# Kernel optimization log

Measured on AMD Instinct MI355X. Metric: run time of the kernel, lower is better.

The kernel has to match this reference:

```python
import jax, jax.numpy as jnp
import numpy as np

EPS = 1e-5

def layer_norm(x, g, b):
    mu = jnp.mean(x, axis=-1, keepdims=True)
    var = jnp.var(x, axis=-1, keepdims=True)
    return (x - mu) * jax.lax.rsqrt(var + EPS) * g + b

def rel_shift(x):
    # x: [N, H, T1, T2] with T2 = 2*T1 - 1 -> [N, H, T1, T1]
    N, H, T1, T2 = x.shape
    zp = jnp.zeros((N, H, T1, 1), dtype=x.dtype)
    xp = jnp.concatenate([zp, x], axis=-1).reshape(N, H, T2 + 1, T1)
    x = xp[:, :, 1:, :].reshape(N, H, T1, T2)
    return x[:, :, :, : T2 // 2 + 1]

def setup_inputs() -> dict:
    B, T, D, Hh = 8, 1024, 512, 8
    dk = D // Hh
    P = 2 * T - 1
    key = jax.random.key(0)
    ks = jax.random.split(key, 12)
    s = 0.02
    return {
        "q": jax.random.normal(ks[0], (B, T, D), jnp.float32),
        "k": jax.random.normal(ks[1], (B, T, D), jnp.float32),
        "v": jax.random.normal(ks[2], (B, T, D), jnp.float32),
        "pos_emb": jax.random.normal(ks[3], (1, P, D), jnp.float32),
        "mask": jnp.ones((B, T, T), jnp.int32),
        "ln_q_g": jnp.ones((D,), jnp.float32), "ln_q_b": jnp.zeros((D,), jnp.float32),
        "ln_k_g": jnp.ones((D,), jnp.float32), "ln_k_b": jnp.zeros((D,), jnp.float32),
        "ln_v_g": jnp.ones((D,), jnp.float32), "ln_v_b": jnp.zeros((D,), jnp.float32),
        "w_q": jax.random.normal(ks[4], (D, D), jnp.float32) * s,   # [out, in]
        "w_k": jax.random.normal(ks[5], (D, D), jnp.float32) * s,
        "w_v": jax.random.normal(ks[6], (D, D), jnp.float32) * s,
        "w_pos": jax.random.normal(ks[7], (D, D), jnp.float32) * s,
        "w_fc": jax.random.normal(ks[8], (D, D), jnp.float32) * s,
        "pos_bias_u": jax.random.normal(ks[9], (Hh, dk), jnp.float32) * s,
        "pos_bias_v": jax.random.normal(ks[10], (Hh, dk), jnp.float32) * s,
    }

def reference(q, k, v, pos_emb, mask, ln_q_g, ln_q_b, ln_k_g, ln_k_b, ln_v_g, ln_v_b,
              w_q, w_k, w_v, w_pos, w_fc, pos_bias_u, pos_bias_v):
    B, T, D = q.shape
    H, dk = pos_bias_u.shape
    scale = 1.0 / np.sqrt(dk).astype(np.float32)
    residual = q
    qn = layer_norm(q, ln_q_g, ln_q_b)
    kn = layer_norm(k, ln_k_g, ln_k_b)
    vn = layer_norm(v, ln_v_g, ln_v_b)
    # projections (torch Linear: x @ W^T), reshape to [B, H, T, dk]
    qh = (qn @ w_q.T).reshape(B, T, H, dk)                      # [B, T, H, dk]
    kh = (kn @ w_k.T).reshape(B, T, H, dk).transpose(0, 2, 1, 3)  # [B, H, T, dk]
    vh = (vn @ w_v.T).reshape(B, T, H, dk).transpose(0, 2, 1, 3)
    p = (pos_emb @ w_pos.T).reshape(pos_emb.shape[0], -1, H, dk).transpose(0, 2, 1, 3)  # [1, H, P, dk]
    q_u = (qh + pos_bias_u).transpose(0, 2, 1, 3)  # [B, H, T, dk]
    q_v = (qh + pos_bias_v).transpose(0, 2, 1, 3)
    matrix_ac = jnp.einsum('bhqd,bhkd->bhqk', q_u, kh)          # [B, H, T, T]
    matrix_bd = jnp.einsum('bhqd,nhpd->bhqp', q_v, p)           # [B, H, T, 2T-1]
    matrix_bd = rel_shift(matrix_bd)                             # [B, H, T, T]
    scores = (matrix_ac + matrix_bd) * scale
    m = (mask[:, None, :, :] == 0)                               # [B, 1, T, T]
    scores = jnp.where(m, -jnp.inf, scores)
    attn = jax.nn.softmax(scores, axis=-1)
    attn = jnp.where(m, 0.0, attn)
    out = jnp.einsum('bhqk,bhkd->bhqd', attn, vh)                # [B, H, T, dk]
    out = out.transpose(0, 2, 1, 3).reshape(B, T, H * dk)
    out = out @ w_fc.T + residual
    return out, attn
```

## Files before the change

### kernel.cpp

```cpp
#include <hip/hip_runtime.h>

constexpr int cT  = 1024;
constexpr int cD  = 512;
constexpr int cDK = 64;
constexpr int cP  = 2047;
constexpr int PBS = 1040;

typedef __attribute__((ext_vector_type(8))) short short8;
typedef __attribute__((ext_vector_type(4))) float floatx4;

#define MFMA16(a,b,c) __builtin_amdgcn_mfma_f32_16x16x32_bf16((a),(b),(c),0,0,0)
#define SWZ(i,j) ((j) ^ ((((i) >> 2) & 3) << 3))

__device__ __forceinline__ void bar_lds(){
  asm volatile("s_waitcnt lgkmcnt(0)\n\ts_barrier" ::: "memory");
}

__device__ __forceinline__ unsigned short f2bf(float f){
  union { float f; unsigned int u; } x; x.f = f;
  unsigned int r = x.u + 0x7fffu + ((x.u >> 16) & 1u);
  return (unsigned short)(r >> 16);
}
__device__ __forceinline__ float bf2f(unsigned short h){
  union { unsigned int u; float f; } x; x.u = ((unsigned int)h) << 16;
  return x.f;
}
__device__ __forceinline__ short8 ld8(const unsigned short* p){
  return *(const short8*)p;
}

struct LN3 { const float* x[3]; const float* g[3]; const float* b[3]; unsigned short* y[3]; };
__global__ void __launch_bounds__(256) ln3_kernel(LN3 a)
{
  __shared__ float red[8];
  const int z = blockIdx.y, r = blockIdx.x;
  const float* x = a.x[z]; const float* g = a.g[z]; const float* b = a.b[z];
  unsigned short* y = a.y[z];
  const float2 v = ((const float2*)(x + (size_t)r * cD))[threadIdx.x];
  float s = v.x + v.y, sq = v.x * v.x + v.y * v.y;
  #pragma unroll
  for (int o = 32; o; o >>= 1){ s += __shfl_xor(s, o); sq += __shfl_xor(sq, o); }
  const int w = threadIdx.x >> 6;
  if ((threadIdx.x & 63) == 0){ red[w * 2] = s; red[w * 2 + 1] = sq; }
  __syncthreads();
  s  = red[0] + red[2] + red[4] + red[6];
  sq = red[1] + red[3] + red[5] + red[7];
  const float mu  = s * (1.0f / cD);
  const float var = sq * (1.0f / cD) - mu * mu;
  const float rs  = rsqrtf(var + 1e-5f);
  const int c = threadIdx.x * 2;
  const unsigned int o0 = f2bf((v.x - mu) * rs * g[c]     + b[c]);
  const unsigned int o1 = f2bf((v.y - mu) * rs * g[c + 1] + b[c + 1]);
  ((unsigned int*)(y + (size_t)r * cD))[threadIdx.x] = o0 | (o1 << 16);
}

struct Ptr5 { const float* p[5]; };
__global__ void __launch_bounds__(256) cast5_kernel(Ptr5 s, unsigned short* __restrict__ d){
  const int idx = blockIdx.x * 256 + threadIdx.x;
  const int seg = idx >> 18, off = idx & 262143;
  d[idx] = f2bf(s.p[seg][off]);
}
__global__ void __launch_bounds__(256) cast1_kernel(const float* __restrict__ s,
    unsigned short* __restrict__ d, int n){
  const int idx = blockIdx.x * 256 + threadIdx.x;
  if (idx < n) d[idx] = f2bf(s[idx]);
}

__global__ void __launch_bounds__(256) maskbits_kernel(
    const int* __restrict__ mask, unsigned int* __restrict__ bm)
{
  const int row = blockIdx.x * 4 + (threadIdx.x >> 6);
  const int lane = threadIdx.x & 63;
  #pragma unroll
  for (int ii = 0; ii < 16; ii++){
    const int m = mask[(size_t)row * cT + ii * 64 + lane];
    const unsigned long long bal = __ballot(m != 0);
    if (lane == 0)       bm[row * 32 + ii * 2]     = (unsigned int)bal;
    else if (lane == 32) bm[row * 32 + ii * 2 + 1] = (unsigned int)(bal >> 32);
  }
}

__global__ void __launch_bounds__(256) gemm512_kernel(
    const unsigned short* __restrict__ A0, const unsigned short* __restrict__ W0,
    int M, int mode, float scaleA, unsigned short* __restrict__ outb,
    float* __restrict__ outf, const float* __restrict__ residual)
{
  const int z = blockIdx.z;
  const unsigned short* A = A0 + (size_t)z * 4194304;
  const unsigned short* W = W0 + (size_t)z * 262144;
  unsigned short* outz = outb ? outb + (size_t)z * 4194304 : outb;
  const float sA = (z == 0) ? scaleA : 1.0f;
  const int n0 = blockIdx.x * 128, m0 = blockIdx.y * 128;
  const int wave = threadIdx.x >> 6, lane = threadIdx.x & 63;
  const int wr = wave >> 1, wc = wave & 1;
  const int l15 = lane & 15, lq = lane >> 4;
  const int mb = m0 + wr * 64, nb = n0 + wc * 64;
  floatx4 acc[4][4];
  #pragma unroll
  for (int i = 0; i < 4; i++)
    #pragma unroll
    for (int j = 0; j < 4; j++) acc[i][j] = (floatx4){0.f, 0.f, 0.f, 0.f};
  for (int k0 = 0; k0 < 512; k0 += 32){
    short8 af[4], bf[4];
    #pragma unroll
    for (int i = 0; i < 4; i++){
      int row = mb + i * 16 + l15; if (row >= M) row = M - 1;
      af[i] = ld8(A + (size_t)row * 512 + k0 + lq * 8);
      const int col = nb + i * 16 + l15;
      bf[i] = ld8(W + (size_t)col * 512 + k0 + lq * 8);
    }
    #pragma unroll
    for (int i = 0; i < 4; i++)
      #pragma unroll
      for (int j = 0; j < 4; j++)
        acc[i][j] = MFMA16(af[i], bf[j], acc[i][j]);
  }
  #pragma unroll
  for (int i = 0; i < 4; i++){
    #pragma unroll
    for (int j = 0; j < 4; j++){
      #pragma unroll
      for (int r = 0; r < 4; r++){
        const int row = mb + i * 16 + lq * 4 + r;
        const int col = nb + j * 16 + l15;
        if (row >= M) continue;
        const float val = acc[i][j][r] * sA;
        if (mode == 0){
          const int bb = row >> 10, t = row & 1023, h = col >> 6, d = col & 63;
          outz[(((size_t)(bb * 8 + h) * 1024 + t) << 6) + d] = f2bf(val);
        } else if (mode == 1){
          const int h = col >> 6, d = col & 63;
          outz[(((size_t)h * 2047 + row) << 6) + d] = f2bf(val);
        } else {
          const size_t idx = (size_t)row * 512 + col;
          outf[idx] = val + residual[idx];
        }
      }
    }
  }
}

__global__ void __launch_bounds__(256) transpose_v_kernel(
    const unsigned short* __restrict__ vh, unsigned short* __restrict__ vt)
{
  __shared__ unsigned short tile[64][65];
  const int bh = blockIdx.x, t0 = blockIdx.y * 64;
  const unsigned short* src = vh + ((size_t)bh * cT + t0) * cDK;
  #pragma unroll
  for (int i = 0; i < 16; i++){
    const int idx = threadIdx.x + i * 256;
    tile[idx >> 6][idx & 63] = src[idx];
  }
  __syncthreads();
  unsigned short* dst = vt + (size_t)bh * cDK * cT + t0;
  #pragma unroll
  for (int i = 0; i < 16; i++){
    const int idx = threadIdx.x + i * 256;
    const int d = idx >> 6, t = idx & 63;
    dst[(size_t)d * cT + t] = tile[t][d];
  }
}

__global__ void __launch_bounds__(256) dot_bias_kernel(
    const unsigned short* __restrict__ X, const float* __restrict__ bias,
    float* __restrict__ out, int rows, int hdiv, float scale)
{
  const int row = blockIdx.x * 4 + (threadIdx.x >> 6);
  const int lane = threadIdx.x & 63;
  if (row >= rows) return;
  const int h = (row / hdiv) & 7;
  float s = bf2f(X[(size_t)row * 64 + lane]) * bias[h * 64 + lane];
  #pragma unroll
  for (int o = 32; o; o >>= 1) s += __shfl_xor(s, o);
  if (lane == 0) out[row] = s * scale;
}

__global__ void __launch_bounds__(512, 4) attn_kernel(
    const unsigned short* __restrict__ qh, const unsigned short* __restrict__ kh,
    const unsigned short* __restrict__ vt, const unsigned short* __restrict__ pproj,
    const float* __restrict__ ubias, const float* __restrict__ vbias,
    const unsigned int* __restrict__ bm, float* __restrict__ attn_out,
    unsigned short* __restrict__ out_h)
{
  __shared__ float sc[16 * cT];
  unsigned short* pbuf = (unsigned short*)sc;
  const int bh = blockIdx.x, b = bh >> 3, h = bh & 7;
  const int q0 = blockIdx.y * 16;
  const int wave = threadIdx.x >> 6, lane = threadIdx.x & 63;
  const int l15 = lane & 15, lq = lane >> 4;
  const unsigned short* Q  = qh + (size_t)bh * cT * cDK;
  const unsigned short* Kp = kh + (size_t)bh * cT * cDK;
  const unsigned short* Pt = pproj + (size_t)h * cP * cDK;
  const float* ub = ubias + (size_t)bh * cT;
  const float* vb = vbias + (size_t)h * cP;

  const short8 qf0 = ld8(Q + (size_t)(q0 + l15) * cDK + lq * 8);
  const short8 qf1 = ld8(Q + (size_t)(q0 + l15) * cDK + 32 + lq * 8);

  for (int jt = wave; jt < 64; jt += 8){
    const short8 kf0 = ld8(Kp + (size_t)(jt * 16 + l15) * cDK + lq * 8);
    const short8 kf1 = ld8(Kp + (size_t)(jt * 16 + l15) * cDK + 32 + lq * 8);
    floatx4 acc = (floatx4){0.f, 0.f, 0.f, 0.f};
    acc = MFMA16(qf0, kf0, acc);
    acc = MFMA16(qf1, kf1, acc);
    const int jb = jt * 16 + l15;
    const float ubv = ub[jb];
    #pragma unroll
    for (int r = 0; r < 4; r++){
      const int i = lq * 4 + r;
      sc[i * cT + (jb ^ (lq << 3))] = acc[r] + ubv + vb[jb + (cT - 1) - (q0 + i)];
    }
  }
  bar_lds();

  const int w0 = (cT - 1) - q0 - 15;
  for (int ct = wave; ct < 65; ct += 8){
    const int c = ct * 16 + l15;
    int prow = w0 + c; if (prow > cP - 1) prow = cP - 1;
    const short8 pf0 = ld8(Pt + (size_t)prow * cDK + lq * 8);
    const short8 pf1 = ld8(Pt + (size_t)prow * cDK + 32 + lq * 8);
    floatx4 acc = (floatx4){0.f, 0.f, 0.f, 0.f};
    acc = MFMA16(qf0, pf0, acc);
    acc = MFMA16(qf1, pf1, acc);
    #pragma unroll
    for (int r = 0; r < 4; r++){
      const int i = lq * 4 + r;
      const int j = c - 15 + i;
      if (j >= 0 && j < cT) sc[i * cT + SWZ(i, j)] += acc[r];
    }
  }
  bar_lds();

  for (int p = 0; p < 2; p++){
    const int i = p * 8 + wave;
    const int qrow = q0 + i;
    const unsigned int* bmr = bm + ((size_t)b * cT + qrow) * 32;
    float vals[16];
    float mx = -INFINITY;
    #pragma unroll
    for (int ii = 0; ii < 16; ii++){
      const int j = lane + ii * 64;
      float s = sc[i * cT + SWZ(i, j)];
      const unsigned int mw = bmr[ii * 2 + (lane >> 5)];
      if (((mw >> (lane & 31)) & 1u) == 0u) s = -INFINITY;
      vals[ii] = s;
      mx = fmaxf(mx, s);
    }
    #pragma unroll
    for (int o = 32; o; o >>= 1) mx = fmaxf(mx, __shfl_xor(mx, o));
    float sum = 0.f;
    #pragma unroll
    for (int ii = 0; ii < 16; ii++){
      const float e = (vals[ii] == -INFINITY) ? 0.f : __expf(vals[ii] - mx);
      vals[ii] = e; sum += e;
    }
    #pragma unroll
    for (int o = 32; o; o >>= 1) sum += __shfl_xor(sum, o);
    const float ri = sum > 0.f ? 1.f / sum : 0.f;
    bar_lds();
    float* arow = attn_out + ((size_t)bh * cT + qrow) * cT;
    #pragma unroll
    for (int ii = 0; ii < 16; ii++){
      const int j = lane + ii * 64;
      const float pr = vals[ii] * ri;
      __builtin_nontemporal_store(pr, arow + j);
      pbuf[i * PBS + j] = f2bf(pr);
    }
  }
  bar_lds();

  const unsigned short* V = vt + (size_t)bh * cDK * cT;
  const int d0 = (wave & 3) * 16;
  const int kh2 = wave >> 2;
  floatx4 acc = (floatx4){0.f, 0.f, 0.f, 0.f};
  for (int ks = 0; ks < 16; ks++){
    const int j0 = (kh2 * 16 + ks) * 32;
    const short8 vf = ld8(V + (size_t)(d0 + l15) * cT + j0 + lq * 8);
    const short8 af = ld8(pbuf + l15 * PBS + j0 + lq * 8);
    acc = MFMA16(af, vf, acc);
  }
  float* red4 = sc + 10240;
  if (kh2 == 1) *(floatx4*)(red4 + ((wave & 3) * 256 + lane * 4)) = acc;
  bar_lds();
  if (kh2 == 0){
    acc += *(const floatx4*)(red4 + ((wave & 3) * 256 + lane * 4));
    #pragma unroll
    for (int r = 0; r < 4; r++){
      const int i = lq * 4 + r;
      out_h[((size_t)b * cT + q0 + i) * cD + h * cDK + d0 + l15] = f2bf(acc[r]);
    }
  }
}

extern "C" void kernel_launch(void* const* d_in, const int* in_sizes, int n_in,
                              void* d_out, int out_size, void* d_ws, size_t ws_size,
                              hipStream_t stream)
{
  const float* q    = (const float*)d_in[0];
  const float* k    = (const float*)d_in[1];
  const float* v    = (const float*)d_in[2];
  const float* pe   = (const float*)d_in[3];
  const int*   mask = (const int*)d_in[4];
  const float* lnqg = (const float*)d_in[5];
  const float* lnqb = (const float*)d_in[6];
  const float* lnkg = (const float*)d_in[7];
  const float* lnkb = (const float*)d_in[8];
  const float* lnvg = (const float*)d_in[9];
  const float* lnvb = (const float*)d_in[10];
  const float* wq   = (const float*)d_in[11];
  const float* wk   = (const float*)d_in[12];
  const float* wv   = (const float*)d_in[13];
  const float* wpos = (const float*)d_in[14];
  const float* wfc  = (const float*)d_in[15];
  const float* pbu  = (const float*)d_in[16];
  const float* pbv  = (const float*)d_in[17];

  float* out_f  = (float*)d_out;
  float* attn_f = out_f + (size_t)8 * 1024 * 512;

  unsigned char* scr = (unsigned char*)attn_f;
  size_t soff = 0;
  auto salloc = [&](size_t bytes){ void* p = scr + soff; soff += (bytes + 255) & ~(size_t)255; return p; };
  unsigned short* qn   = (unsigned short*)salloc((size_t)8192 * 512 * 2);
  unsigned short* kn   = (unsigned short*)salloc((size_t)8192 * 512 * 2);
  unsigned short* vn   = (unsigned short*)salloc((size_t)8192 * 512 * 2);
  unsigned short* pe_b = (unsigned short*)salloc((size_t)2047 * 512 * 2);
  (void)kn; (void)vn;

  unsigned char* ws = (unsigned char*)d_ws;
  size_t off = 0;
  auto alloc = [&](size_t bytes){ void* p = ws + off; off += (bytes + 255) & ~(size_t)255; return p; };
  unsigned short* w5_b = (unsigned short*)alloc(5 * 512 * 512 * 2);
  unsigned short* qhb  = (unsigned short*)alloc((size_t)8192 * 512 * 2);
  unsigned short* khb  = (unsigned short*)alloc((size_t)8192 * 512 * 2);
  unsigned short* vhb  = (unsigned short*)alloc((size_t)8192 * 512 * 2);
  unsigned short* vtb  = (unsigned short*)alloc((size_t)8192 * 512 * 2);
  unsigned short* ppb  = (unsigned short*)alloc((size_t)8 * 2047 * 64 * 2);
  float*          ub   = (float*)alloc((size_t)8 * 8 * 1024 * 4);
  float*          vbias= (float*)alloc((size_t)8 * 2047 * 4);
  unsigned short* ohb  = (unsigned short*)alloc((size_t)8192 * 512 * 2);
  unsigned int*   bmask= (unsigned int*)alloc((size_t)8192 * 32 * 4);
  (void)ws_size; (void)n_in; (void)in_sizes; (void)out_size;

  Ptr5 c5; c5.p[0] = wq; c5.p[1] = wk; c5.p[2] = wv; c5.p[3] = wpos; c5.p[4] = wfc;
  cast5_kernel<<<5120, 256, 0, stream>>>(c5, w5_b);
  cast1_kernel<<<4094, 256, 0, stream>>>(pe, pe_b, 2047 * 512);
  maskbits_kernel<<<2048, 256, 0, stream>>>(mask, bmask);

  LN3 l3;
  l3.x[0] = q; l3.x[1] = k; l3.x[2] = v;
  l3.g[0] = lnqg; l3.g[1] = lnkg; l3.g[2] = lnvg;
  l3.b[0] = lnqb; l3.b[1] = lnkb; l3.b[2] = lnvb;
  l3.y[0] = qn; l3.y[1] = kn; l3.y[2] = vn;
  ln3_kernel<<<dim3(8192, 3), 256, 0, stream>>>(l3);

  gemm512_kernel<<<dim3(4, 64, 3), 256, 0, stream>>>(qn, w5_b, 8192, 0, 0.125f,
                                                     qhb, nullptr, nullptr);
  gemm512_kernel<<<dim3(4, 16, 1), 256, 0, stream>>>(pe_b, w5_b + 3 * 262144, 2047, 1, 1.0f,
                                                     ppb, nullptr, nullptr);

  transpose_v_kernel<<<dim3(64, 16), 256, 0, stream>>>(vhb, vtb);

  dot_bias_kernel<<<16384, 256, 0, stream>>>(khb, pbu, ub, 65536, 1024, 0.125f);
  dot_bias_kernel<<<4094, 256, 0, stream>>>(ppb, pbv, vbias, 16376, 2047, 0.125f);

  attn_kernel<<<dim3(64, 64), 512, 0, stream>>>(qhb, khb, vtb, ppb, ub, vbias,
                                                bmask, attn_f, ohb);

  gemm512_kernel<<<dim3(4, 64, 1), 256, 0, stream>>>(ohb, w5_b + 4 * 262144, 8192, 2, 1.0f,
                                                     nullptr, out_f, q);
}
```

Before: 722.1 us.

## Vectorize softmax LDS/global access, prefetch V fragments, unroll score loops

The softmax phase now reads four scores per lane as a float4 from swizzled LDS, stores attention probabilities with 128-bit nontemporal stores and writes packed bf16 quads into the P buffer. This replaces the previous scalar per-element access. Half of the V fragments are loaded into registers before softmax so that global latency overlaps with the softmax work. The QK and positional loops are fully unrolled, with the leftover 65th position tile peeled onto wave 0, and the projection GEMM gets a launch-bounds occupancy hint and an unroll-2 pragma. The costs are more register pressure from the prefetched fragments and possible spilling under the new launch bound.

Measured after the change: 686.5 us. -4.9%, faster.

```diff
diff --git a/kernel.cpp b/kernel.cpp
--- a/kernel.cpp
+++ b/kernel.cpp
@@ -80,7 +80,7 @@
   }
 }
 
-__global__ void __launch_bounds__(256) gemm512_kernel(
+__global__ void __launch_bounds__(256, 4) gemm512_kernel(
     const unsigned short* __restrict__ A0, const unsigned short* __restrict__ W0,
     int M, int mode, float scaleA, unsigned short* __restrict__ outb,
     float* __restrict__ outf, const float* __restrict__ residual)
@@ -100,6 +100,7 @@
   for (int i = 0; i < 4; i++)
     #pragma unroll
     for (int j = 0; j < 4; j++) acc[i][j] = (floatx4){0.f, 0.f, 0.f, 0.f};
+  #pragma unroll 2
   for (int k0 = 0; k0 < 512; k0 += 32){
     short8 af[4], bf[4];
     #pragma unroll
@@ -197,7 +198,9 @@
   const short8 qf0 = ld8(Q + (size_t)(q0 + l15) * cDK + lq * 8);
   const short8 qf1 = ld8(Q + (size_t)(q0 + l15) * cDK + 32 + lq * 8);
 
-  for (int jt = wave; jt < 64; jt += 8){
+  #pragma unroll
+  for (int t = 0; t < 8; t++){
+    const int jt = wave + t * 8;
     const short8 kf0 = ld8(Kp + (size_t)(jt * 16 + l15) * cDK + lq * 8);
     const short8 kf1 = ld8(Kp + (size_t)(jt * 16 + l15) * cDK + 32 + lq * 8);
     floatx4 acc = (floatx4){0.f, 0.f, 0.f, 0.f};
@@ -214,7 +217,9 @@
   bar_lds();
 
   const int w0 = (cT - 1) - q0 - 15;
-  for (int ct = wave; ct < 65; ct += 8){
+  #pragma unroll
+  for (int t = 0; t < 8; t++){
+    const int ct = wave + t * 8;
     const int c = ct * 16 + l15;
     int prow = w0 + c; if (prow > cP - 1) prow = cP - 1;
     const short8 pf0 = ld8(Pt + (size_t)prow * cDK + lq * 8);
@@ -229,22 +234,52 @@
       if (j >= 0 && j < cT) sc[i * cT + SWZ(i, j)] += acc[r];
     }
   }
+  if (wave == 0){
+    const int c = 1024 + l15;
+    int prow = w0 + c; if (prow > cP - 1) prow = cP - 1;
+    const short8 pf0 = ld8(Pt + (size_t)prow * cDK + lq * 8);
+    const short8 pf1 = ld8(Pt + (size_t)prow * cDK + 32 + lq * 8);
+    floatx4 acc = (floatx4){0.f, 0.f, 0.f, 0.f};
+    acc = MFMA16(qf0, pf0, acc);
+    acc = MFMA16(qf1, pf1, acc);
+    #pragma unroll
+    for (int r = 0; r < 4; r++){
+      const int i = lq * 4 + r;
+      const int j = c - 15 + i;
+      if (j >= 0 && j < cT) sc[i * cT + SWZ(i, j)] += acc[r];
+    }
+  }
   bar_lds();
+
+  const unsigned short* V = vt + (size_t)bh * cDK * cT;
+  const int d0 = (wave & 3) * 16;
+  const int kh2 = wave >> 2;
+  short8 vfr[8];
+  #pragma unroll
+  for (int ks = 0; ks < 8; ks++){
+    const int j0v = (kh2 * 16 + ks) * 32;
+    vfr[ks] = ld8(V + (size_t)(d0 + l15) * cT + j0v + lq * 8);
+  }
 
   for (int p = 0; p < 2; p++){
     const int i = p * 8 + wave;
     const int qrow = q0 + i;
     const unsigned int* bmr = bm + ((size_t)b * cT + qrow) * 32;
+    const int xr = ((i >> 2) & 3) << 3;
     float vals[16];
     float mx = -INFINITY;
     #pragma unroll
-    for (int ii = 0; ii < 16; ii++){
-      const int j = lane + ii * 64;
-      float s = sc[i * cT + SWZ(i, j)];
-      const unsigned int mw = bmr[ii * 2 + (lane >> 5)];
-      if (((mw >> (lane & 31)) & 1u) == 0u) s = -INFINITY;
-      vals[ii] = s;
-      mx = fmaxf(mx, s);
+    for (int ii = 0; ii < 4; ii++){
+      const int j0 = lane * 4 + ii * 256;
+      const unsigned int mw = bmr[(lane >> 3) + ii * 8] >> (4 * (lane & 7));
+      const floatx4 sv = *(const floatx4*)&sc[i * cT + (j0 ^ xr)];
+      #pragma unroll
+      for (int tt = 0; tt < 4; tt++){
+        float s = sv[tt];
+        if (((mw >> tt) & 1u) == 0u) s = -INFINITY;
+        vals[ii * 4 + tt] = s;
+        mx = fmaxf(mx, s);
+      }
     }
     #pragma unroll
     for (int o = 32; o; o >>= 1) mx = fmaxf(mx, __shfl_xor(mx, o));
@@ -259,21 +294,31 @@
     const float ri = sum > 0.f ? 1.f / sum : 0.f;
     bar_lds();
     float* arow = attn_out + ((size_t)bh * cT + qrow) * cT;
-    #pragma unroll
-    for (int ii = 0; ii < 16; ii++){
-      const int j = lane + ii * 64;
-      const float pr = vals[ii] * ri;
-      __builtin_nontemporal_store(pr, arow + j);
-      pbuf[i * PBS + j] = f2bf(pr);
+    unsigned short* prow_lds = pbuf + (size_t)i * PBS;
+    #pragma unroll
+    for (int ii = 0; ii < 4; ii++){
+      const int j0 = lane * 4 + ii * 256;
+      floatx4 pv;
+      #pragma unroll
+      for (int tt = 0; tt < 4; tt++) pv[tt] = vals[ii * 4 + tt] * ri;
+      __builtin_nontemporal_store(pv, (floatx4*)(arow + j0));
+      const unsigned int wlo = (unsigned int)f2bf(pv[0]) | ((unsigned int)f2bf(pv[1]) << 16);
+      const unsigned int whi = (unsigned int)f2bf(pv[2]) | ((unsigned int)f2bf(pv[3]) << 16);
+      *(unsigned long long*)(prow_lds + j0) =
+          (unsigned long long)wlo | ((unsigned long long)whi << 32);
     }
   }
   bar_lds();
 
-  const unsigned short* V = vt + (size_t)bh * cDK * cT;
-  const int d0 = (wave & 3) * 16;
-  const int kh2 = wave >> 2;
   floatx4 acc = (floatx4){0.f, 0.f, 0.f, 0.f};
-  for (int ks = 0; ks < 16; ks++){
+  #pragma unroll
+  for (int ks = 0; ks < 8; ks++){
+    const int j0 = (kh2 * 16 + ks) * 32;
+    const short8 af = ld8(pbuf + l15 * PBS + j0 + lq * 8);
+    acc = MFMA16(af, vfr[ks], acc);
+  }
+  #pragma unroll
+  for (int ks = 8; ks < 16; ks++){
     const int j0 = (kh2 * 16 + ks) * 32;
     const short8 vf = ld8(V + (size_t)(d0 + l15) * cT + j0 + lq * 8);
     const short8 af = ld8(pbuf + l15 * PBS + j0 + lq * 8);
```
